# Optimization experiments

Hardware: AMD Instinct MI355X
Metric: run time of the kernel (lower is better)

The kernel has to match this reference:

```python
import jax, jax.numpy as jnp
import numpy as np

B, S, D = 2, 2048, 1024
H = 16
HD = D // H  # 64


def setup_inputs() -> dict:
    key = jax.random.key(0)
    ks = jax.random.split(key, 6)
    std = 1.0 / np.sqrt(D)
    x = jax.random.normal(ks[0], (B, S, D), dtype=jnp.float32)
    Wq = jax.random.uniform(ks[1], (D, D), jnp.float32, -std, std)
    Wk = jax.random.uniform(ks[2], (D, D), jnp.float32, -std, std)
    Wv = jax.random.uniform(ks[3], (D, D), jnp.float32, -std, std)
    Wo = jax.random.uniform(ks[4], (D, D), jnp.float32, -std, std)
    bo = jax.random.uniform(ks[5], (D,), jnp.float32, -std, std)
    return {"x": x, "Wq": Wq, "Wk": Wk, "Wv": Wv, "Wo": Wo, "bo": bo}


def reference(x, Wq, Wk, Wv, Wo, bo):
    b, n, _ = x.shape
    # project and split heads: [b, H, n, HD]
    def split_heads(y):
        return y.reshape(b, n, H, HD).transpose(0, 2, 1, 3)
    q = split_heads(jnp.einsum('bnd,ed->bne', x, Wq))
    k = split_heads(jnp.einsum('bnd,ed->bne', x, Wk))
    v = split_heads(jnp.einsum('bnd,ed->bne', x, Wv))
    scores = jnp.einsum('bhqd,bhkd->bhqk', q, k)
    causal = jnp.triu(jnp.ones((n, n), dtype=bool), k=1)
    # original masks with -inf BEFORE scaling; -inf/scale == -inf so math matches
    scores = jnp.where(causal, -jnp.inf, scores) / jnp.sqrt(jnp.asarray(HD, scores.dtype))
    attn = jax.nn.softmax(scores, axis=-1)
    ctx = jnp.einsum('bhqk,bhkd->bhqd', attn, v)
    ctx = ctx.transpose(0, 2, 1, 3).reshape(b, n, D)
    return jnp.einsum('bnd,ed->bne', ctx, Wo) + bo
```

## Files before the change

### kernel.cpp

```cpp
#include <hip/hip_runtime.h>

#define DEV __device__ __forceinline__

typedef __bf16 bf16x8 __attribute__((ext_vector_type(8)));
typedef float f32x4 __attribute__((ext_vector_type(4)));
typedef float f32x16 __attribute__((ext_vector_type(16)));
typedef unsigned u32x4 __attribute__((ext_vector_type(4)));

constexpr int S_LEN = 2048;
constexpr int DMODEL = 1024;
constexpr int NHEAD = 16;
constexpr int HDIM = 64;
constexpr int BATCH = 2;
constexpr int MROWS = BATCH * S_LEN;
constexpr float QSCALE = 0.125f * 1.44269504088896f;

DEV short f2bf(float x) {
  unsigned u = __builtin_bit_cast(unsigned, x);
  unsigned r = u + 0x7fffu + ((u >> 16) & 1u);
  return (short)(r >> 16);
}

#define MFMA16(a, b, c) __builtin_amdgcn_mfma_f32_16x16x32_bf16((a), (b), (c), 0, 0, 0)
#define MFMA32(a, b, c) __builtin_amdgcn_mfma_f32_32x32x16_bf16((a), (b), (c), 0, 0, 0)
#define GLL16(g, l)                                                                     \
  __builtin_amdgcn_global_load_lds((const __attribute__((address_space(1))) void*)(g),  \
                                   (__attribute__((address_space(3))) void*)(l), 16, 0, 0)

DEV unsigned cvt_pk_bf16(float a, float b) {
  unsigned r;
  asm("v_cvt_pk_bf16_f32 %0, %1, %2" : "=v"(r) : "v"(a), "v"(b));
  return r;
}
DEV void swap32(unsigned& a, unsigned& b) {
  asm("v_permlane32_swap_b32 %0, %1" : "+v"(a), "+v"(b));
}

__global__ void cvt_all(const float* __restrict__ x, const float* __restrict__ wq,
                        const float* __restrict__ wk, const float* __restrict__ wv,
                        const float* __restrict__ wo, short* __restrict__ out) {
  const size_t XNe = (size_t)MROWS * DMODEL;
  const size_t WNe = (size_t)DMODEL * DMODEL;
  const size_t tot = XNe + 4 * WNe;
  size_t i = ((size_t)blockIdx.x * blockDim.x + threadIdx.x) * 4;
  const size_t stride = (size_t)gridDim.x * blockDim.x * 4;
  for (; i < tot; i += stride) {
    const float* src;
    size_t off;
    if (i < XNe) {
      src = x;
      off = i;
    } else {
      const size_t k = i - XNe;
      const int seg = (int)(k >> 20);
      off = k & (WNe - 1);
      src = seg == 0 ? wq : seg == 1 ? wk : seg == 2 ? wv : wo;
    }
    float4 v = *(const float4*)&src[off];
    short4 r;
    r.x = f2bf(v.x);
    r.y = f2bf(v.y);
    r.z = f2bf(v.z);
    r.w = f2bf(v.w);
    *(short4*)&out[i] = r;
  }
}

__global__ __launch_bounds__(256) void gemm_bt(const short* __restrict__ A,
                                               const short* __restrict__ Bt,
                                               short* __restrict__ outb) {
  constexpr int K = DMODEL;
  constexpr size_t XN = (size_t)MROWS * DMODEL;
  __shared__ short As[2][128 * 64];
  __shared__ short Bs[2][128 * 64];
  const int tid = threadIdx.x;
  const int w = tid >> 6, l = tid & 63;
  const int lr = l & 15, lh = l >> 4;
  const int wr = w >> 1, wc = w & 1;
  const int tm = blockIdx.x, tn = blockIdx.y;
  const bool vswap = (tn >= 16);

  const int srow = tid >> 3;
  const int ssl = tid & 7;
  const int ssg = ssl ^ (srow & 7);

  f32x4 acc[4][4] = {};

#define GSTAGE(KT, BUF)                                                             \
  {                                                                                 \
    _Pragma("unroll") for (int i = 0; i < 4; ++i) {                                 \
      const int row = i * 32 + srow;                                                \
      GLL16(A + (size_t)(tm * 128 + row) * K + (KT)*64 + ssg * 8,                   \
            &As[BUF][(i * 256 + w * 64) * 8]);                                      \
    }                                                                               \
    _Pragma("unroll") for (int i = 0; i < 4; ++i) {                                 \
      const int row = i * 32 + srow;                                                \
      GLL16(Bt + (size_t)(tn * 128 + row) * K + (KT)*64 + ssg * 8,                  \
            &Bs[BUF][(i * 256 + w * 64) * 8]);                                      \
    }                                                                               \
  }

  GSTAGE(0, 0);
  asm volatile("s_waitcnt vmcnt(0)" ::: "memory");
  __syncthreads();

  for (int kt = 0; kt < K / 64; ++kt) {
    const int buf = kt & 1;
    if (kt < K / 64 - 1) GSTAGE(kt + 1, buf ^ 1);

#pragma unroll
    for (int kh = 0; kh < 2; ++kh) {
      bf16x8 af[4], bfr[4];
#pragma unroll
      for (int mi = 0; mi < 4; ++mi) {
        const int row = wr * 64 + mi * 16 + lr;
        af[mi] = *(const bf16x8*)&As[buf][row * 64 + 8 * ((kh * 4 + lh) ^ (row & 7))];
      }
#pragma unroll
      for (int ni = 0; ni < 4; ++ni) {
        const int row = wc * 64 + ni * 16 + lr;
        bfr[ni] = *(const bf16x8*)&Bs[buf][row * 64 + 8 * ((kh * 4 + lh) ^ (row & 7))];
      }
      if (vswap) {
#pragma unroll
        for (int mi = 0; mi < 4; ++mi)
#pragma unroll
          for (int ni = 0; ni < 4; ++ni)
            acc[mi][ni] = MFMA16(bfr[ni], af[mi], acc[mi][ni]);
      } else {
#pragma unroll
        for (int mi = 0; mi < 4; ++mi)
#pragma unroll
          for (int ni = 0; ni < 4; ++ni)
            acc[mi][ni] = MFMA16(af[mi], bfr[ni], acc[mi][ni]);
      }
    }

    asm volatile("s_waitcnt vmcnt(0)" ::: "memory");
    __syncthreads();
  }
#undef GSTAGE

  const int m0 = tm * 128 + wr * 64;
  const int n0 = tn * 128 + wc * 64;
  if (vswap) {
#pragma unroll
    for (int mi = 0; mi < 4; ++mi)
#pragma unroll
      for (int ni = 0; ni < 4; ++ni)
#pragma unroll
        for (int i = 0; i < 4; ++i) {
          const int e = n0 + ni * 16 + lh * 4 + i;
          const int m = m0 + mi * 16 + lr;
          const int ecol = e & (DMODEL - 1);
          const int b = m >> 11, n = m & (S_LEN - 1);
          const int h = ecol >> 6, d = ecol & (HDIM - 1);
          (outb + 2 * XN)[((size_t)((b * NHEAD + h) * HDIM + d)) * S_LEN + n] =
              f2bf(acc[mi][ni][i]);
        }
  } else {
    const int sel = tn >> 3;
#pragma unroll
    for (int mi = 0; mi < 4; ++mi)
#pragma unroll
      for (int ni = 0; ni < 4; ++ni)
#pragma unroll
        for (int i = 0; i < 4; ++i) {
          const int m = m0 + mi * 16 + lh * 4 + i;
          const int e = n0 + ni * 16 + lr;
          const int ecol = e & (DMODEL - 1);
          const int b = m >> 11, n = m & (S_LEN - 1);
          const int h = ecol >> 6, d = ecol & (HDIM - 1);
          if (sel == 0)
            outb[((size_t)((b * NHEAD + h) * S_LEN + n)) * HDIM + d] =
                f2bf(acc[mi][ni][i] * QSCALE);
          else
            (outb + XN)[((size_t)((b * NHEAD + h) * S_LEN + n)) * HDIM + d] =
                f2bf(acc[mi][ni][i]);
        }
  }
}

__global__ __launch_bounds__(256) void gemm_out(const short* __restrict__ A,
                                                const short* __restrict__ Bt,
                                                float* __restrict__ outf,
                                                const float* __restrict__ bias) {
  constexpr int K = DMODEL;
  constexpr int N = DMODEL;
  __shared__ short As[2][64 * 64];
  __shared__ short Bs[2][64 * 64];
  const int tid = threadIdx.x;
  const int w = tid >> 6, l = tid & 63;
  const int lr = l & 15, lh = l >> 4;
  const int wr = w >> 1, wc = w & 1;
  const int tm = blockIdx.x, tn = blockIdx.y;

  const int srow = tid >> 3;
  const int ssl = tid & 7;
  const int ssg = ssl ^ (srow & 7);

  f32x4 acc[2][2] = {};

#define OSTAGE(KT, BUF)                                                             \
  {                                                                                 \
    _Pragma("unroll") for (int i = 0; i < 2; ++i) {                                 \
      const int row = i * 32 + srow;                                                \
      GLL16(A + (size_t)(tm * 64 + row) * K + (KT)*64 + ssg * 8,                    \
            &As[BUF][(i * 256 + w * 64) * 8]);                                      \
    }                                                                               \
    _Pragma("unroll") for (int i = 0; i < 2; ++i) {                                 \
      const int row = i * 32 + srow;                                                \
      GLL16(Bt + (size_t)(tn * 64 + row) * K + (KT)*64 + ssg * 8,                   \
            &Bs[BUF][(i * 256 + w * 64) * 8]);                                      \
    }                                                                               \
  }

  OSTAGE(0, 0);
  asm volatile("s_waitcnt vmcnt(0)" ::: "memory");
  __syncthreads();

  for (int kt = 0; kt < K / 64; ++kt) {
    const int buf = kt & 1;
    if (kt < K / 64 - 1) OSTAGE(kt + 1, buf ^ 1);

#pragma unroll
    for (int kh = 0; kh < 2; ++kh) {
      bf16x8 af[2], bfr[2];
#pragma unroll
      for (int mi = 0; mi < 2; ++mi) {
        const int row = wr * 32 + mi * 16 + lr;
        af[mi] = *(const bf16x8*)&As[buf][row * 64 + 8 * ((kh * 4 + lh) ^ (row & 7))];
      }
#pragma unroll
      for (int ni = 0; ni < 2; ++ni) {
        const int row = wc * 32 + ni * 16 + lr;
        bfr[ni] = *(const bf16x8*)&Bs[buf][row * 64 + 8 * ((kh * 4 + lh) ^ (row & 7))];
      }
#pragma unroll
      for (int mi = 0; mi < 2; ++mi)
#pragma unroll
        for (int ni = 0; ni < 2; ++ni)
          acc[mi][ni] = MFMA16(af[mi], bfr[ni], acc[mi][ni]);
    }

    asm volatile("s_waitcnt vmcnt(0)" ::: "memory");
    __syncthreads();
  }
#undef OSTAGE

#pragma unroll
  for (int mi = 0; mi < 2; ++mi)
#pragma unroll
    for (int ni = 0; ni < 2; ++ni)
#pragma unroll
      for (int i = 0; i < 2 * 2; ++i) {
        const int m = tm * 64 + wr * 32 + mi * 16 + lh * 4 + i;
        const int e = tn * 64 + wc * 32 + ni * 16 + lr;
        outf[(size_t)m * N + e] = acc[mi][ni][i] + bias[e];
      }
}

__global__ __launch_bounds__(256) void attn_kernel(const short* __restrict__ Qg,
                                                   const short* __restrict__ Kg,
                                                   const short* __restrict__ Vg,
                                                   short* __restrict__ ctx) {
  __shared__ alignas(16) short KV[4][8192];
  __shared__ float mls[4][2][32];
  const int tidx = threadIdx.x;
  const int s = tidx >> 6;
  const int l = tidx & 63;
  const int lq = l & 31;
  const int h5 = l >> 5;
  const int bid = blockIdx.x;
  const int xcd = bid & 7;
  const int j = bid >> 3;
  const int bh = xcd * 4 + (j >> 5);
  const int qc = 31 - (j & 31);
  const int qbase = qc * 64;
  const short* Qh = Qg + (size_t)bh * (S_LEN * HDIM);
  const short* Kh = Kg + (size_t)bh * (S_LEN * HDIM);
  const short* Vh = Vg + (size_t)bh * (HDIM * S_LEN);

  short* Kbase = &KV[s][0];
  short* Vbase = &KV[s][4096];
  const int r8 = l >> 3;
  const int sc = l & 7;

  bf16x8 qf0[4], qf1[4];
#pragma unroll
  for (int cc = 0; cc < 4; ++cc) {
    qf0[cc] = *(const bf16x8*)&Qh[(size_t)(qbase + lq) * HDIM + cc * 16 + h5 * 8];
    qf1[cc] = *(const bf16x8*)&Qh[(size_t)(qbase + 32 + lq) * HDIM + cc * 16 + h5 * 8];
  }

  f32x16 o00 = {}, o01 = {}, o10 = {}, o11 = {};
  float ll0 = 0.f, ll1 = 0.f;

  const int ntot = 2 * qc + 2;
  const int td0 = 2 * qc, td1 = 2 * qc + 1;
  const int ts = (ntot * s) >> 2;
  const int te = (ntot * (s + 1)) >> 2;

#define STAGE(T, BUF)                                                              \
  {                                                                                \
    _Pragma("unroll") for (int i = 0; i < 4; ++i) {                                \
      const int R = i * 8 + r8;                                                    \
      const int sg = sc ^ (R & 7);                                                 \
      GLL16(Kh + (size_t)((T)*32 + R) * HDIM + sg * 8,                             \
            &Kbase[(BUF)*2048 + i * 512]);                                         \
      GLL16(Vh + (size_t)(2 * R + (sg >> 2)) * S_LEN + (T)*32 + (sg & 3) * 8,      \
            &Vbase[(BUF)*2048 + i * 512]);                                         \
    }                                                                              \
  }

  if (ts < te) STAGE(ts, 0);

  for (int t = ts; t < te; ++t) {
    const int buf = (t - ts) & 1;
    if (t + 1 < te) {
      STAGE(t + 1, buf ^ 1);
      asm volatile("s_waitcnt vmcnt(8)" ::: "memory");
    } else {
      asm volatile("s_waitcnt vmcnt(0)" ::: "memory");
    }
    const short* Ksb = &Kbase[buf * 2048];
    const short* Vsb = &Vbase[buf * 2048];

    bf16x8 kf[4];
#pragma unroll
    for (int cc = 0; cc < 4; ++cc)
      kf[cc] = *(const bf16x8*)&Ksb[lq * 64 + 8 * ((cc * 2 + h5) ^ (lq & 7))];
    const int R0 = lq >> 1, p0 = (lq & 1) * 4 + h5;
    const int R1 = 16 + (lq >> 1);
    const bf16x8 v00 = *(const bf16x8*)&Vsb[R0 * 64 + 8 * ((p0 + 0) ^ (R0 & 7))];
    const bf16x8 v01 = *(const bf16x8*)&Vsb[R0 * 64 + 8 * ((p0 + 2) ^ (R0 & 7))];
    const bf16x8 v10 = *(const bf16x8*)&Vsb[R1 * 64 + 8 * ((p0 + 0) ^ (R1 & 7))];
    const bf16x8 v11 = *(const bf16x8*)&Vsb[R1 * 64 + 8 * ((p0 + 2) ^ (R1 & 7))];

    f32x16 st0 = {}, st1 = {};
    __builtin_amdgcn_s_setprio(1);
#pragma unroll
    for (int cc = 0; cc < 4; ++cc) {
      st0 = MFMA32(kf[cc], qf0[cc], st0);
      st1 = MFMA32(kf[cc], qf1[cc], st1);
    }
    __builtin_amdgcn_s_setprio(0);

    if (t == td0) {
#pragma unroll
      for (int rr = 0; rr < 16; ++rr) {
        const int crow = (rr & 3) + 8 * (rr >> 2) + 4 * h5;
        if (crow > lq) st0[rr] = -__builtin_inff();
      }
    } else if (t == td1) {
#pragma unroll
      for (int rr = 0; rr < 16; ++rr) {
        st0[rr] = -__builtin_inff();
        const int crow = (rr & 3) + 8 * (rr >> 2) + 4 * h5;
        if (crow > lq) st1[rr] = -__builtin_inff();
      }
    }

#pragma unroll
    for (int rr = 0; rr < 16; ++rr) st0[rr] = __builtin_amdgcn_exp2f(st0[rr]);
#pragma unroll
    for (int rr = 0; rr < 16; ++rr) st1[rr] = __builtin_amdgcn_exp2f(st1[rr]);
    {
      const float a = ((st0[0] + st0[1]) + (st0[2] + st0[3])) +
                      ((st0[4] + st0[5]) + (st0[6] + st0[7]));
      const float b = ((st0[8] + st0[9]) + (st0[10] + st0[11])) +
                      ((st0[12] + st0[13]) + (st0[14] + st0[15]));
      ll0 += a + b;
      const float c = ((st1[0] + st1[1]) + (st1[2] + st1[3])) +
                      ((st1[4] + st1[5]) + (st1[6] + st1[7]));
      const float d = ((st1[8] + st1[9]) + (st1[10] + st1[11])) +
                      ((st1[12] + st1[13]) + (st1[14] + st1[15]));
      ll1 += c + d;
    }

    unsigned a0 = cvt_pk_bf16(st0[0], st0[1]), b0 = cvt_pk_bf16(st0[4], st0[5]);
    unsigned a1 = cvt_pk_bf16(st0[2], st0[3]), b1 = cvt_pk_bf16(st0[6], st0[7]);
    unsigned a2 = cvt_pk_bf16(st0[8], st0[9]), b2 = cvt_pk_bf16(st0[12], st0[13]);
    unsigned a3 = cvt_pk_bf16(st0[10], st0[11]), b3 = cvt_pk_bf16(st0[14], st0[15]);
    unsigned c0 = cvt_pk_bf16(st1[0], st1[1]), d0 = cvt_pk_bf16(st1[4], st1[5]);
    unsigned c1 = cvt_pk_bf16(st1[2], st1[3]), d1 = cvt_pk_bf16(st1[6], st1[7]);
    unsigned c2 = cvt_pk_bf16(st1[8], st1[9]), d2 = cvt_pk_bf16(st1[12], st1[13]);
    unsigned c3 = cvt_pk_bf16(st1[10], st1[11]), d3 = cvt_pk_bf16(st1[14], st1[15]);
    swap32(a0, b0);
    swap32(a1, b1);
    swap32(a2, b2);
    swap32(a3, b3);
    swap32(c0, d0);
    swap32(c1, d1);
    swap32(c2, d2);
    swap32(c3, d3);
    const u32x4 pwA0 = {a0, a1, b0, b1};
    const u32x4 pwA1 = {a2, a3, b2, b3};
    const u32x4 pwB0 = {c0, c1, d0, d1};
    const u32x4 pwB1 = {c2, c3, d2, d3};
    const bf16x8 pa0 = __builtin_bit_cast(bf16x8, pwA0);
    const bf16x8 pa1 = __builtin_bit_cast(bf16x8, pwA1);
    const bf16x8 pb0 = __builtin_bit_cast(bf16x8, pwB0);
    const bf16x8 pb1 = __builtin_bit_cast(bf16x8, pwB1);

    __builtin_amdgcn_s_setprio(1);
    o00 = MFMA32(pa0, v00, o00);
    o10 = MFMA32(pb0, v00, o10);
    o01 = MFMA32(pa0, v10, o01);
    o11 = MFMA32(pb0, v10, o11);
    o00 = MFMA32(pa1, v01, o00);
    o10 = MFMA32(pb1, v01, o10);
    o01 = MFMA32(pa1, v11, o01);
    o11 = MFMA32(pb1, v11, o11);
    __builtin_amdgcn_s_setprio(0);
  }
#undef STAGE

  float* me = (float*)&KV[s][0];
#pragma unroll
  for (int rr = 0; rr < 16; ++rr) {
    const int crow = (rr & 3) + 8 * (rr >> 2) + 4 * h5;
    me[crow * 64 + lq] = o00[rr];
    me[crow * 64 + 32 + lq] = o01[rr];
    me[(32 + crow) * 64 + lq] = o10[rr];
    me[(32 + crow) * 64 + 32 + lq] = o11[rr];
  }
  ll0 += __shfl_xor(ll0, 32);
  ll1 += __shfl_xor(ll1, 32);
  if (h5 == 0) {
    mls[s][0][lq] = ll0;
    mls[s][1][lq] = ll1;
  }
  __syncthreads();

  const float* om = (const float*)&KV[0][0];
  const int b = bh >> 4, h = bh & (NHEAD - 1);
  const int r2 = tidx >> 2;
  const int d0 = (tidx & 3) * 16;
  const float lsum = mls[0][r2 >> 5][r2 & 31] + mls[1][r2 >> 5][r2 & 31] +
                     mls[2][r2 >> 5][r2 & 31] + mls[3][r2 >> 5][r2 & 31];
  const float inv = __builtin_amdgcn_rcpf(lsum);
  const size_t base = (size_t)(b * S_LEN + qbase + r2) * DMODEL + h * HDIM + d0;
#pragma unroll
  for (int i = 0; i < 16; ++i) {
    const int o = r2 * 64 + d0 + i;
    const float v = om[o] + om[4096 + o] + om[8192 + o] + om[12288 + o];
    ctx[base + i] = f2bf(v * inv);
  }
}

extern "C" void kernel_launch(void* const* d_in, const int* in_sizes, int n_in,
                              void* d_out, int out_size, void* d_ws, size_t ws_size,
                              hipStream_t stream) {
  const float* x = (const float*)d_in[0];
  const float* Wq = (const float*)d_in[1];
  const float* Wk = (const float*)d_in[2];
  const float* Wv = (const float*)d_in[3];
  const float* Wo = (const float*)d_in[4];
  const float* bo = (const float*)d_in[5];

  const size_t XN = (size_t)MROWS * DMODEL;
  const size_t WN = (size_t)DMODEL * DMODEL;

  short* ws = (short*)d_ws;
  short* xb = ws;
  short* Wqb = xb + XN;
  short* Wob = Wqb + 3 * WN;
  short* Qb = Wob + WN;
  short* Kb = Qb + XN;
  short* Vb = Kb + XN;
  short* ctxb = Vb + XN;
  if (ws_size < (5 * XN + 4 * WN) * sizeof(short)) return;

  cvt_all<<<2048, 256, 0, stream>>>(x, Wq, Wk, Wv, Wo, xb);

  gemm_bt<<<dim3(MROWS / 128, 3 * DMODEL / 128), 256, 0, stream>>>(xb, Wqb, Qb);

  attn_kernel<<<1024, 256, 0, stream>>>(Qb, Kb, Vb, ctxb);

  gemm_out<<<dim3(MROWS / 64, DMODEL / 64), 256, 0, stream>>>(ctxb, Wob, (float*)d_out,
                                                              bo);
}
```

Before: 114.6 us.

## Rewrite QKV GEMM as 256x256-tile 8-wave kernel with interleaved staging

Replaces the 128x128 four-wave QKV projection GEMM with a 256x256-tile, 512-thread kernel in which each wave computes a 128x64 sub-tile. Global-to-LDS loads for the next K step are split into quarters and interleaved with four MFMA phases, using partial vmcnt waits and raw barriers plus setprio around MFMA blocks. The aim is more data reuse per tile and better overlap of memory loads with compute. In exchange the kernel uses 128 KB of LDS and more accumulator registers, and launches only 192 blocks, which may leave some compute units idle.

```diff
diff --git a/kernel.cpp b/kernel.cpp
--- a/kernel.cpp
+++ b/kernel.cpp
@@ -66,117 +66,175 @@
   }
 }
 
-__global__ __launch_bounds__(256) void gemm_bt(const short* __restrict__ A,
-                                               const short* __restrict__ Bt,
-                                               short* __restrict__ outb) {
+__global__ __launch_bounds__(512) void gemm_qkv8(const short* __restrict__ A,
+                                                 const short* __restrict__ Bt,
+                                                 short* __restrict__ outb) {
   constexpr int K = DMODEL;
+  constexpr int NT = K / 64;
   constexpr size_t XN = (size_t)MROWS * DMODEL;
-  __shared__ short As[2][128 * 64];
-  __shared__ short Bs[2][128 * 64];
+  __shared__ short Alds[2][256 * 64];
+  __shared__ short Blds[2][256 * 64];
   const int tid = threadIdx.x;
   const int w = tid >> 6, l = tid & 63;
   const int lr = l & 15, lh = l >> 4;
-  const int wr = w >> 1, wc = w & 1;
+  const int wm = w >> 2, wn = w & 3;
   const int tm = blockIdx.x, tn = blockIdx.y;
-  const bool vswap = (tn >= 16);
-
-  const int srow = tid >> 3;
-  const int ssl = tid & 7;
-  const int ssg = ssl ^ (srow & 7);
-
-  f32x4 acc[4][4] = {};
-
-#define GSTAGE(KT, BUF)                                                             \
-  {                                                                                 \
-    _Pragma("unroll") for (int i = 0; i < 4; ++i) {                                 \
-      const int row = i * 32 + srow;                                                \
-      GLL16(A + (size_t)(tm * 128 + row) * K + (KT)*64 + ssg * 8,                   \
-            &As[BUF][(i * 256 + w * 64) * 8]);                                      \
-    }                                                                               \
-    _Pragma("unroll") for (int i = 0; i < 4; ++i) {                                 \
-      const int row = i * 32 + srow;                                                \
-      GLL16(Bt + (size_t)(tn * 128 + row) * K + (KT)*64 + ssg * 8,                  \
-            &Bs[BUF][(i * 256 + w * 64) * 8]);                                      \
-    }                                                                               \
-  }
-
-  GSTAGE(0, 0);
-  asm volatile("s_waitcnt vmcnt(0)" ::: "memory");
-  __syncthreads();
-
-  for (int kt = 0; kt < K / 64; ++kt) {
-    const int buf = kt & 1;
-    if (kt < K / 64 - 1) GSTAGE(kt + 1, buf ^ 1);
-
-#pragma unroll
-    for (int kh = 0; kh < 2; ++kh) {
-      bf16x8 af[4], bfr[4];
-#pragma unroll
-      for (int mi = 0; mi < 4; ++mi) {
-        const int row = wr * 64 + mi * 16 + lr;
-        af[mi] = *(const bf16x8*)&As[buf][row * 64 + 8 * ((kh * 4 + lh) ^ (row & 7))];
-      }
-#pragma unroll
-      for (int ni = 0; ni < 4; ++ni) {
-        const int row = wc * 64 + ni * 16 + lr;
-        bfr[ni] = *(const bf16x8*)&Bs[buf][row * 64 + 8 * ((kh * 4 + lh) ^ (row & 7))];
-      }
-      if (vswap) {
-#pragma unroll
-        for (int mi = 0; mi < 4; ++mi)
-#pragma unroll
-          for (int ni = 0; ni < 4; ++ni)
-            acc[mi][ni] = MFMA16(bfr[ni], af[mi], acc[mi][ni]);
-      } else {
-#pragma unroll
-        for (int mi = 0; mi < 4; ++mi)
-#pragma unroll
-          for (int ni = 0; ni < 4; ++ni)
-            acc[mi][ni] = MFMA16(af[mi], bfr[ni], acc[mi][ni]);
-      }
-    }
-
+  const bool vswap = (tn >= 8);
+
+  const int l3 = l >> 3;
+  const int scol = ((l & 7) ^ l3) * 8;
+
+  f32x4 acc[8][4] = {};
+  bf16x8 af[8], bfv[4];
+
+#define STAGE_A(KT2, NB, H)                                                   \
+  {                                                                           \
+    _Pragma("unroll") for (int i = 0; i < 2; ++i) {                           \
+      const int r = w * 8 + l3 + i * 128 + (H)*64;                            \
+      GLL16(A + (size_t)(tm * 256 + r) * K + (KT2)*64 + scol,                 \
+            &Alds[NB][(i * 1024 + (H)*512 + w * 64) * 8]);                    \
+    }                                                                         \
+  }
+#define STAGE_B(KT2, NB, J)                                                   \
+  {                                                                           \
+    _Pragma("unroll") for (int i = 0; i < 2; ++i) {                           \
+      const int g = i * 2 + (w >> 2);                                         \
+      const int r = g * 64 + (J)*32 + (w & 3) * 8 + l3;                       \
+      GLL16(Bt + (size_t)(tn * 256 + r) * K + (KT2)*64 + scol,                \
+            &Blds[NB][(g * 512 + (J)*256 + (w & 3) * 64) * 8]);               \
+    }                                                                         \
+  }
+
+#define RD_A(BUF, MH)                                                          \
+  _Pragma("unroll") for (int mi = 0; mi < 4; ++mi) {                           \
+    const int r = wm * 128 + (MH)*64 + mi * 16 + lr;                           \
+    af[mi * 2 + 0] = *(const bf16x8*)&Alds[BUF][r * 64 + 8 * (lh ^ (r & 7))];  \
+    af[mi * 2 + 1] =                                                           \
+        *(const bf16x8*)&Alds[BUF][r * 64 + 8 * ((4 + lh) ^ (r & 7))];         \
+  }
+#define RD_B(BUF, NH)                                                          \
+  _Pragma("unroll") for (int ni = 0; ni < 2; ++ni) {                           \
+    const int r = wn * 64 + (NH)*32 + ni * 16 + lr;                            \
+    bfv[ni * 2 + 0] = *(const bf16x8*)&Blds[BUF][r * 64 + 8 * (lh ^ (r & 7))]; \
+    bfv[ni * 2 + 1] =                                                          \
+        *(const bf16x8*)&Blds[BUF][r * 64 + 8 * ((4 + lh) ^ (r & 7))];         \
+  }
+
+#define MM(MH, NH)                                                             \
+  {                                                                            \
+    __builtin_amdgcn_s_setprio(1);                                             \
+    if (!vswap) {                                                              \
+      _Pragma("unroll") for (int ks = 0; ks < 2; ++ks)                         \
+      _Pragma("unroll") for (int mi = 0; mi < 4; ++mi)                         \
+      _Pragma("unroll") for (int ni = 0; ni < 2; ++ni)                         \
+          acc[(MH)*4 + mi][(NH)*2 + ni] = MFMA16(                              \
+              af[mi * 2 + ks], bfv[ni * 2 + ks], acc[(MH)*4 + mi][(NH)*2 + ni]); \
+    } else {                                                                   \
+      _Pragma("unroll") for (int ks = 0; ks < 2; ++ks)                         \
+      _Pragma("unroll") for (int mi = 0; mi < 4; ++mi)                         \
+      _Pragma("unroll") for (int ni = 0; ni < 2; ++ni)                         \
+          acc[(MH)*4 + mi][(NH)*2 + ni] = MFMA16(                              \
+              bfv[ni * 2 + ks], af[mi * 2 + ks], acc[(MH)*4 + mi][(NH)*2 + ni]); \
+    }                                                                          \
+    __builtin_amdgcn_s_setprio(0);                                             \
+  }
+
+#define BARR()                       \
+  __builtin_amdgcn_s_barrier();      \
+  asm volatile("" ::: "memory")
+#define VW4() asm volatile("s_waitcnt vmcnt(4)" ::: "memory")
+
+  STAGE_A(0, 0, 0);
+  STAGE_B(0, 0, 0);
+  STAGE_B(0, 0, 1);
+  STAGE_A(0, 0, 1);
+
+  for (int kt = 0; kt < NT - 1; ++kt) {
+    const int buf = kt & 1, nb = buf ^ 1;
+    VW4();
+    BARR();
+    RD_A(buf, 0);
+    RD_B(buf, 0);
+    STAGE_A(kt + 1, nb, 0);
+    MM(0, 0);
+    VW4();
+    BARR();
+    RD_B(buf, 1);
+    STAGE_B(kt + 1, nb, 0);
+    MM(0, 1);
+    VW4();
+    BARR();
+    RD_A(buf, 1);
+    RD_B(buf, 0);
+    STAGE_B(kt + 1, nb, 1);
+    MM(1, 0);
+    BARR();
+    RD_B(buf, 1);
+    STAGE_A(kt + 1, nb, 1);
+    MM(1, 1);
+  }
+  {
+    const int buf = (NT - 1) & 1;
+    VW4();
+    BARR();
+    RD_A(buf, 0);
+    RD_B(buf, 0);
+    MM(0, 0);
+    asm volatile("s_waitcnt vmcnt(2)" ::: "memory");
+    BARR();
+    RD_B(buf, 1);
+    MM(0, 1);
     asm volatile("s_waitcnt vmcnt(0)" ::: "memory");
-    __syncthreads();
-  }
-#undef GSTAGE
-
-  const int m0 = tm * 128 + wr * 64;
-  const int n0 = tn * 128 + wc * 64;
-  if (vswap) {
-#pragma unroll
-    for (int mi = 0; mi < 4; ++mi)
+    BARR();
+    RD_A(buf, 1);
+    RD_B(buf, 0);
+    MM(1, 0);
+    BARR();
+    RD_B(buf, 1);
+    MM(1, 1);
+  }
+#undef STAGE_A
+#undef STAGE_B
+#undef RD_A
+#undef RD_B
+#undef MM
+#undef BARR
+#undef VW4
+
+  const int m0 = tm * 256 + wm * 128;
+  const int e0 = (tn & 3) * 256 + wn * 64;
+  const int sel = tn >> 2;
+  if (sel == 2) {
+#pragma unroll
+    for (int mi = 0; mi < 8; ++mi)
 #pragma unroll
       for (int ni = 0; ni < 4; ++ni)
 #pragma unroll
-        for (int i = 0; i < 4; ++i) {
-          const int e = n0 + ni * 16 + lh * 4 + i;
+        for (int ii = 0; ii < 4; ++ii) {
+          const int e = e0 + ni * 16 + lh * 4 + ii;
           const int m = m0 + mi * 16 + lr;
-          const int ecol = e & (DMODEL - 1);
           const int b = m >> 11, n = m & (S_LEN - 1);
-          const int h = ecol >> 6, d = ecol & (HDIM - 1);
+          const int h = e >> 6, d = e & (HDIM - 1);
           (outb + 2 * XN)[((size_t)((b * NHEAD + h) * HDIM + d)) * S_LEN + n] =
-              f2bf(acc[mi][ni][i]);
+              f2bf(acc[mi][ni][ii]);
         }
   } else {
-    const int sel = tn >> 3;
-#pragma unroll
-    for (int mi = 0; mi < 4; ++mi)
+#pragma unroll
+    for (int mi = 0; mi < 8; ++mi)
 #pragma unroll
       for (int ni = 0; ni < 4; ++ni)
 #pragma unroll
-        for (int i = 0; i < 4; ++i) {
-          const int m = m0 + mi * 16 + lh * 4 + i;
-          const int e = n0 + ni * 16 + lr;
-          const int ecol = e & (DMODEL - 1);
+        for (int ii = 0; ii < 4; ++ii) {
+          const int m = m0 + mi * 16 + lh * 4 + ii;
+          const int e = e0 + ni * 16 + lr;
           const int b = m >> 11, n = m & (S_LEN - 1);
-          const int h = ecol >> 6, d = ecol & (HDIM - 1);
+          const int h = e >> 6, d = e & (HDIM - 1);
           if (sel == 0)
             outb[((size_t)((b * NHEAD + h) * S_LEN + n)) * HDIM + d] =
-                f2bf(acc[mi][ni][i] * QSCALE);
+                f2bf(acc[mi][ni][ii] * QSCALE);
           else
             (outb + XN)[((size_t)((b * NHEAD + h) * S_LEN + n)) * HDIM + d] =
-                f2bf(acc[mi][ni][i]);
+                f2bf(acc[mi][ni][ii]);
         }
   }
 }
@@ -474,7 +532,7 @@
 
   cvt_all<<<2048, 256, 0, stream>>>(x, Wq, Wk, Wv, Wo, xb);
 
-  gemm_bt<<<dim3(MROWS / 128, 3 * DMODEL / 128), 256, 0, stream>>>(xb, Wqb, Qb);
+  gemm_qkv8<<<dim3(MROWS / 256, 3 * DMODEL / 256), 512, 0, stream>>>(xb, Wqb, Qb);
 
   attn_kernel<<<1024, 256, 0, stream>>>(Qb, Kb, Vb, ctxb);
 
```

New measurement: 113.5 us. No clear change (-0.9%).
